# Performance work log

Hardware: AMD Instinct MI355X
Metric: run time of the kernel (lower is better)

The kernel has to match this reference:

```python
import jax, jax.numpy as jnp
import numpy as np
from jax import lax

H = W = 1024

def _conv_sig(x, w, b):
    # 3x3 conv, padding=1 (SAME), NCHW / OIHW, followed by sigmoid
    y = lax.conv_general_dilated(x, w, (1, 1), 'SAME',
                                 dimension_numbers=('NCHW', 'OIHW', 'NCHW'))
    return jax.nn.sigmoid(y + b[None, :, None, None])


def setup_inputs() -> dict:
    key = jax.random.key(0)
    ks = jax.random.split(key, 20)
    d = {
        'x':  jax.random.normal(ks[0], (1, 3, H, W), jnp.float32),
        'x2': jax.random.normal(ks[1], (1, 3, H, W), jnp.float32),
        'w1a': jax.random.normal(ks[2], (1, 3, 3, 3), jnp.float32) * 0.1,
        'b1a': jax.random.normal(ks[3], (1,), jnp.float32) * 0.1,
        'w2a': jax.random.normal(ks[4], (1, 4, 3, 3), jnp.float32) * 0.1,
        'b2a': jax.random.normal(ks[5], (1,), jnp.float32) * 0.1,
        'w3a': jax.random.normal(ks[6], (1, 5, 3, 3), jnp.float32) * 0.1,
        'b3a': jax.random.normal(ks[7], (1,), jnp.float32) * 0.1,
        'w1b': jax.random.normal(ks[8], (1, 3, 3, 3), jnp.float32) * 0.1,
        'b1b': jax.random.normal(ks[9], (1,), jnp.float32) * 0.1,
        'w2b': jax.random.normal(ks[10], (1, 4, 3, 3), jnp.float32) * 0.1,
        'b2b': jax.random.normal(ks[11], (1,), jnp.float32) * 0.1,
        'w3b': jax.random.normal(ks[12], (1, 5, 3, 3), jnp.float32) * 0.1,
        'b3b': jax.random.normal(ks[13], (1,), jnp.float32) * 0.1,
        'lw1': jax.random.normal(ks[14], (128, 6), jnp.float32) * 0.1,
        'lb1': jax.random.normal(ks[15], (128,), jnp.float32) * 0.1,
        'lw2': jax.random.normal(ks[16], (2, 128), jnp.float32) * 0.1,
        'lb2': jax.random.normal(ks[17], (2,), jnp.float32) * 0.1,
    }
    return d


def _encode(x, params):
    # three stacked conv(3x3)+sigmoid blocks with densenet-style concat: C 3->4->5->6
    (w1, b1), (w2, b2), (w3, b3) = params
    x = jnp.concatenate([x, _conv_sig(x, w1, b1)], axis=1)
    x = jnp.concatenate([x, _conv_sig(x, w2, b2)], axis=1)
    x = jnp.concatenate([x, _conv_sig(x, w3, b3)], axis=1)
    return x  # [1, 6, H, W]


def reference(x, x2, w1a, b1a, w2a, b2a, w3a, b3a,
              w1b, b1b, w2b, b2b, w3b, b3b, lw1, lb1, lw2, lb2):
    # name branch: passthrough (3-channel input, e.g. name='opt')
    xa = _encode(x,  [(w1a, b1a), (w2a, b2a), (w3a, b3a)])
    xb = _encode(x2, [(w1b, b1b), (w2b, b2b), (w3b, b3b)])
    x3 = xa - xb                                   # [1, 6, H, W]
    feat = jnp.transpose(x3, (0, 2, 3, 1)).reshape(H * W, 6)
    feat = feat @ lw1.T + lb1                      # [HW, 128]
    outfeature = feat @ lw2.T + lb2                # [HW, 2]
    den_x1 = jnp.transpose(xa, (0, 2, 3, 1)).reshape(H, W, 6)
    den_x2 = jnp.transpose(xb, (0, 2, 3, 1)).reshape(H, W, 6)
    return outfeature, den_x1, den_x2
```

## Files before the change

### kernel.cpp

```cpp
#include <hip/hip_runtime.h>
#include <math.h>

#define IMG  1024
#define TS   32
#define HALO 3
#define XT   38
#define S1T  36
#define S2T  34

__device__ __forceinline__ float sigf(float y) {
    return 1.0f / (1.0f + __expf(-y));
}

__device__ __forceinline__ void acc9(float acc[4], const float v[6][3], const float* w9) {
#pragma unroll
    for (int dy = 0; dy < 3; ++dy)
#pragma unroll
        for (int dx = 0; dx < 3; ++dx) {
            float ww = w9[dy * 3 + dx];
#pragma unroll
            for (int rr = 0; rr < 4; ++rr)
                acc[rr] += ww * v[rr + dy][dx];
        }
}

__global__ __launch_bounds__(256, 4)
void unet_fused(const float* __restrict__ x, const float* __restrict__ x2,
                const float* __restrict__ w1a, const float* __restrict__ b1a,
                const float* __restrict__ w2a, const float* __restrict__ b2a,
                const float* __restrict__ w3a, const float* __restrict__ b3a,
                const float* __restrict__ w1b, const float* __restrict__ b1b,
                const float* __restrict__ w2b, const float* __restrict__ b2b,
                const float* __restrict__ w3b, const float* __restrict__ b3b,
                const float* __restrict__ lw1, const float* __restrict__ lb1,
                const float* __restrict__ lw2, const float* __restrict__ lb2,
                float* __restrict__ out)
{
    __shared__ float xt[3][XT * XT];
    __shared__ float s1[S1T * S1T];
    __shared__ float s2[S2T * S2T];
    __shared__ float wc[14];

    const int tid = threadIdx.x;
    const int bx = blockIdx.x, by = blockIdx.y;
    const int row0 = by * TS - HALO, col0 = bx * TS - HALO;

    const int c_out = tid & 31;
    const int r0_out = (tid >> 5) * 4;

    if (tid < 12) {
        int o = tid / 6, ch = tid % 6;
        float acc = 0.0f;
        for (int k = 0; k < 128; ++k) acc += lw2[o * 128 + k] * lw1[k * 6 + ch];
        wc[tid] = acc;
    } else if (tid < 14) {
        int o = tid - 12;
        float acc = lb2[o];
        for (int k = 0; k < 128; ++k) acc += lw2[o * 128 + k] * lb1[k];
        wc[tid] = acc;
    }

    const float* XS[2] = {x, x2};
    const float* W1[2] = {w1a, w1b};
    const float* W2[2] = {w2a, w2b};
    const float* W3[2] = {w3a, w3b};
    const float* B1[2] = {b1a, b1b};
    const float* B2[2] = {b2a, b2b};
    const float* B3[2] = {b3a, b3b};

    const long out1 = (long)2 * IMG * IMG;
    const long out2 = out1 + (long)6 * IMG * IMG;

    float areg[4][6];

#pragma unroll
    for (int br = 0; br < 2; ++br) {
        const float* xin = XS[br];
        for (int idx = tid; idx < 3 * XT * XT; idx += 256) {
            int pl = idx / (XT * XT);
            int i  = idx - pl * (XT * XT);
            int r = i / XT, cc = i - r * XT;
            int gr = row0 + r, gc = col0 + cc;
            bool ok = ((unsigned)gr < (unsigned)IMG) && ((unsigned)gc < (unsigned)IMG);
            float v = 0.0f;
            if (ok) v = xin[(long)pl * (IMG * IMG) + (long)gr * IMG + gc];
            xt[pl][i] = v;
        }
        __syncthreads();

        {
            float w[27];
#pragma unroll
            for (int i = 0; i < 27; ++i) w[i] = W1[br][i];
            const float bias = B1[br][0];
            for (int item = tid; item < S1T * 9; item += 256) {
                int c = item % S1T, rg = item / S1T;
                int r0 = rg * 4;
                float acc[4] = {bias, bias, bias, bias};
#pragma unroll
                for (int ic = 0; ic < 3; ++ic) {
                    const float* xp = &xt[ic][r0 * XT + c];
                    float v[6][3];
#pragma unroll
                    for (int rr = 0; rr < 6; ++rr)
#pragma unroll
                        for (int cc = 0; cc < 3; ++cc)
                            v[rr][cc] = xp[rr * XT + cc];
                    acc9(acc, v, &w[ic * 9]);
                }
                int gc1 = col0 + 1 + c;
                bool cok = (unsigned)gc1 < (unsigned)IMG;
                float* so = &s1[r0 * S1T + c];
#pragma unroll
                for (int rr = 0; rr < 4; ++rr) {
                    int gr1 = row0 + 1 + r0 + rr;
                    bool ok = cok && ((unsigned)gr1 < (unsigned)IMG);
                    so[rr * S1T] = ok ? sigf(acc[rr]) : 0.0f;
                }
            }
        }
        __syncthreads();

        {
            float w[36];
#pragma unroll
            for (int i = 0; i < 36; ++i) w[i] = W2[br][i];
            const float bias = B2[br][0];
            for (int item = tid; item < S2T * 9; item += 256) {
                int c = item % S2T, rg = item / S2T;
                int r0 = rg * 4;
                float acc[4] = {bias, bias, bias, bias};
#pragma unroll
                for (int ic = 0; ic < 3; ++ic) {
                    float v[6][3];
#pragma unroll
                    for (int rr = 0; rr < 6; ++rr) {
                        int rrow = r0 + 1 + rr; if (rrow > XT - 1) rrow = XT - 1;
#pragma unroll
                        for (int cc = 0; cc < 3; ++cc)
                            v[rr][cc] = xt[ic][rrow * XT + (c + 1 + cc)];
                    }
                    acc9(acc, v, &w[ic * 9]);
                }
                {
                    float v[6][3];
#pragma unroll
                    for (int rr = 0; rr < 6; ++rr) {
                        int rrow = r0 + rr; if (rrow > S1T - 1) rrow = S1T - 1;
#pragma unroll
                        for (int cc = 0; cc < 3; ++cc)
                            v[rr][cc] = s1[rrow * S1T + (c + cc)];
                    }
                    acc9(acc, v, &w[27]);
                }
                int gc2 = col0 + 2 + c;
                bool cok = (unsigned)gc2 < (unsigned)IMG;
                float* so = &s2[r0 * S2T + c];
#pragma unroll
                for (int rr = 0; rr < 4; ++rr) {
                    int srow = r0 + rr;
                    if (srow < S2T) {
                        int gr2 = row0 + 2 + srow;
                        bool ok = cok && ((unsigned)gr2 < (unsigned)IMG);
                        so[rr * S2T] = ok ? sigf(acc[rr]) : 0.0f;
                    }
                }
            }
        }
        __syncthreads();

        {
            float w[45];
#pragma unroll
            for (int i = 0; i < 45; ++i) w[i] = W3[br][i];
            const float bias = B3[br][0];
            const int c = c_out, r0 = r0_out;
            float acc[4] = {bias, bias, bias, bias};
#pragma unroll
            for (int ic = 0; ic < 3; ++ic) {
                float v[6][3];
#pragma unroll
                for (int rr = 0; rr < 6; ++rr)
#pragma unroll
                    for (int cc = 0; cc < 3; ++cc)
                        v[rr][cc] = xt[ic][(r0 + 2 + rr) * XT + (c + 2 + cc)];
                acc9(acc, v, &w[ic * 9]);
            }
            {
                float v[6][3];
#pragma unroll
                for (int rr = 0; rr < 6; ++rr)
#pragma unroll
                    for (int cc = 0; cc < 3; ++cc)
                        v[rr][cc] = s1[(r0 + 1 + rr) * S1T + (c + 1 + cc)];
                acc9(acc, v, &w[27]);
            }
            {
                float v[6][3];
#pragma unroll
                for (int rr = 0; rr < 6; ++rr)
#pragma unroll
                    for (int cc = 0; cc < 3; ++cc)
                        v[rr][cc] = s2[(r0 + rr) * S2T + (c + cc)];
                acc9(acc, v, &w[36]);
            }

            float cur[4][6];
#pragma unroll
            for (int rr = 0; rr < 4; ++rr) {
#pragma unroll
                for (int ch = 0; ch < 3; ++ch)
                    cur[rr][ch] = xt[ch][(r0 + 3 + rr) * XT + (c + 3)];
                cur[rr][3] = s1[(r0 + 2 + rr) * S1T + (c + 2)];
                cur[rr][4] = s2[(r0 + 1 + rr) * S2T + (c + 1)];
                cur[rr][5] = sigf(acc[rr]);
            }

            const long denOff = (br == 0) ? out1 : out2;
#pragma unroll
            for (int rr = 0; rr < 4; ++rr) {
                long gr = (long)by * TS + r0 + rr;
                long pix = gr * IMG + ((long)bx * TS + c);
                float* pd = out + denOff + pix * 6;
#pragma unroll
                for (int ch = 0; ch < 6; ++ch) pd[ch] = cur[rr][ch];
            }

            if (br == 0) {
#pragma unroll
                for (int rr = 0; rr < 4; ++rr)
#pragma unroll
                    for (int ch = 0; ch < 6; ++ch) areg[rr][ch] = cur[rr][ch];
            } else {
                float wcr[14];
#pragma unroll
                for (int i = 0; i < 14; ++i) wcr[i] = wc[i];
#pragma unroll
                for (int rr = 0; rr < 4; ++rr) {
                    float o0 = wcr[12], o1 = wcr[13];
#pragma unroll
                    for (int ch = 0; ch < 6; ++ch) {
                        float d = areg[rr][ch] - cur[rr][ch];
                        o0 += wcr[ch]     * d;
                        o1 += wcr[6 + ch] * d;
                    }
                    long gr = (long)by * TS + r0 + rr;
                    long pix = gr * IMG + ((long)bx * TS + c);
                    out[pix * 2]     = o0;
                    out[pix * 2 + 1] = o1;
                }
            }
        }
        __syncthreads();
    }
}

extern "C" void kernel_launch(void* const* d_in, const int* in_sizes, int n_in,
                              void* d_out, int out_size, void* d_ws, size_t ws_size,
                              hipStream_t stream) {
    const float* x   = (const float*)d_in[0];
    const float* x2  = (const float*)d_in[1];
    const float* w1a = (const float*)d_in[2];
    const float* b1a = (const float*)d_in[3];
    const float* w2a = (const float*)d_in[4];
    const float* b2a = (const float*)d_in[5];
    const float* w3a = (const float*)d_in[6];
    const float* b3a = (const float*)d_in[7];
    const float* w1b = (const float*)d_in[8];
    const float* b1b = (const float*)d_in[9];
    const float* w2b = (const float*)d_in[10];
    const float* b2b = (const float*)d_in[11];
    const float* w3b = (const float*)d_in[12];
    const float* b3b = (const float*)d_in[13];
    const float* lw1 = (const float*)d_in[14];
    const float* lb1 = (const float*)d_in[15];
    const float* lw2 = (const float*)d_in[16];
    const float* lb2 = (const float*)d_in[17];
    float* out = (float*)d_out;

    dim3 grid(IMG / TS, IMG / TS);
    unet_fused<<<grid, 256, 0, stream>>>(x, x2,
                                         w1a, b1a, w2a, b2a, w3a, b3a,
                                         w1b, b1b, w2b, b2b, w3b, b3b,
                                         lw1, lb1, lw2, lb2, out);
}
```

Before: 155.7 us.

## Give each wavefront private conv1/conv2 halo tiles to drop block barriers

Each of the four wavefronts now computes its own 12-row conv1 and 10-row conv2 strips, with the halo rows recomputed, in per-wave shared buffers. This removes the block-wide __syncthreads between the conv stages. The convs now use a sliding row window that reuses each loaded row across three output rows instead of reloading 6x3 patches. The branch-0 features are reduced straight to the two projected partial sums, which frees registers. The cost is redundant halo compute and idle lanes: only 36 and 34 of the 64 lanes are active in stages 1 and 2.

```diff
diff --git a/kernel.cpp b/kernel.cpp
--- a/kernel.cpp
+++ b/kernel.cpp
@@ -1,28 +1,17 @@
 #include <hip/hip_runtime.h>
-#include <math.h>
 
 #define IMG  1024
 #define TS   32
-#define HALO 3
 #define XT   38
-#define S1T  36
-#define S2T  34
-
-__device__ __forceinline__ float sigf(float y) {
-    return 1.0f / (1.0f + __expf(-y));
-}
-
-__device__ __forceinline__ void acc9(float acc[4], const float v[6][3], const float* w9) {
-#pragma unroll
-    for (int dy = 0; dy < 3; ++dy)
-#pragma unroll
-        for (int dx = 0; dx < 3; ++dx) {
-            float ww = w9[dy * 3 + dx];
-#pragma unroll
-            for (int rr = 0; rr < 4; ++rr)
-                acc[rr] += ww * v[rr + dy][dx];
-        }
-}
+#define XTA  (XT*XT)
+#define S1R  12
+#define S1C  36
+#define S2R  10
+#define S2C  34
+#define OUT1 (2*IMG*IMG)
+#define OUT2 (OUT1 + 6*IMG*IMG)
+
+__device__ __forceinline__ float sigf(float y) { return 1.0f / (1.0f + __expf(-y)); }
 
 __global__ __launch_bounds__(256, 4)
 void unet_fused(const float* __restrict__ x, const float* __restrict__ x2,
@@ -36,20 +25,18 @@
                 const float* __restrict__ lw2, const float* __restrict__ lb2,
                 float* __restrict__ out)
 {
-    __shared__ float xt[3][XT * XT];
-    __shared__ float s1[S1T * S1T];
-    __shared__ float s2[S2T * S2T];
+    __shared__ float xt[3][XTA];
+    __shared__ float s1[4][S1R * S1C];
+    __shared__ float s2[4][S2R * S2C];
     __shared__ float wc[14];
 
-    const int tid = threadIdx.x;
-    const int bx = blockIdx.x, by = blockIdx.y;
-    const int row0 = by * TS - HALO, col0 = bx * TS - HALO;
-
-    const int c_out = tid & 31;
-    const int r0_out = (tid >> 5) * 4;
+    const int tid  = threadIdx.x;
+    const int wv   = tid >> 6;
+    const int lane = tid & 63;
+    const int R0 = blockIdx.y * TS, C0 = blockIdx.x * TS;
 
     if (tid < 12) {
-        int o = tid / 6, ch = tid % 6;
+        int o = tid / 6, ch = tid - o * 6;
         float acc = 0.0f;
         for (int k = 0; k < 128; ++k) acc += lw2[o * 128 + k] * lw1[k * 6 + ch];
         wc[tid] = acc;
@@ -68,190 +55,217 @@
     const float* B2[2] = {b2a, b2b};
     const float* B3[2] = {b3a, b3b};
 
-    const long out1 = (long)2 * IMG * IMG;
-    const long out2 = out1 + (long)6 * IMG * IMG;
-
-    float areg[4][6];
+    float pa[4][2];
+    float* s1w = s1[wv];
+    float* s2w = s2[wv];
+
+    const int c_out = lane & 31;
+    const int rg    = lane >> 5;
+    const int tr0   = 8 * wv + rg * 4;
 
 #pragma unroll
     for (int br = 0; br < 2; ++br) {
+        __syncthreads();
         const float* xin = XS[br];
-        for (int idx = tid; idx < 3 * XT * XT; idx += 256) {
-            int pl = idx / (XT * XT);
-            int i  = idx - pl * (XT * XT);
-            int r = i / XT, cc = i - r * XT;
-            int gr = row0 + r, gc = col0 + cc;
-            bool ok = ((unsigned)gr < (unsigned)IMG) && ((unsigned)gc < (unsigned)IMG);
+        for (int it = tid; it < 3 * XTA; it += 256) {
+            int ch = it / XTA, rem = it - ch * XTA;
+            int r = rem / XT, c = rem - r * XT;
+            int gr = R0 - 3 + r, gc = C0 - 3 + c;
             float v = 0.0f;
-            if (ok) v = xin[(long)pl * (IMG * IMG) + (long)gr * IMG + gc];
-            xt[pl][i] = v;
+            if ((unsigned)gr < (unsigned)IMG && (unsigned)gc < (unsigned)IMG)
+                v = xin[ch * (IMG * IMG) + gr * IMG + gc];
+            xt[ch][rem] = v;
         }
         __syncthreads();
 
+        if (lane < S1C) {
+            const int sc = lane;
+            const float b1 = B1[br][0];
+            float acc[S1R];
+#pragma unroll
+            for (int q = 0; q < S1R; ++q) acc[q] = b1;
+#pragma unroll
+            for (int ch = 0; ch < 3; ++ch) {
+                float w9[9];
+#pragma unroll
+                for (int i = 0; i < 9; ++i) w9[i] = W1[br][ch * 9 + i];
+                const float* xp = &xt[ch][(8 * wv) * XT + sc];
+#pragma unroll
+                for (int r = 0; r < 14; ++r) {
+                    float a0 = xp[0], a1 = xp[1], a2 = xp[2];
+                    xp += XT;
+#pragma unroll
+                    for (int dy = 0; dy < 3; ++dy) {
+                        int q = r - dy;
+                        if (q >= 0 && q < S1R)
+                            acc[q] += w9[dy * 3] * a0 + w9[dy * 3 + 1] * a1 + w9[dy * 3 + 2] * a2;
+                    }
+                }
+            }
+            const int gcol = C0 - 2 + sc;
+            const bool cok = (unsigned)gcol < (unsigned)IMG;
+            const int grow0 = R0 + 8 * wv - 2;
+#pragma unroll
+            for (int q = 0; q < S1R; ++q) {
+                bool ok = cok && ((unsigned)(grow0 + q) < (unsigned)IMG);
+                s1w[q * S1C + sc] = ok ? sigf(acc[q]) : 0.0f;
+            }
+        }
+
+        if (lane < S2C) {
+            const int sc = lane;
+            const float b2 = B2[br][0];
+            float acc[S2R];
+#pragma unroll
+            for (int q = 0; q < S2R; ++q) acc[q] = b2;
+#pragma unroll
+            for (int ch = 0; ch < 3; ++ch) {
+                float w9[9];
+#pragma unroll
+                for (int i = 0; i < 9; ++i) w9[i] = W2[br][ch * 9 + i];
+                const float* xp = &xt[ch][(8 * wv + 1) * XT + (sc + 1)];
+#pragma unroll
+                for (int r = 0; r < 12; ++r) {
+                    float a0 = xp[0], a1 = xp[1], a2 = xp[2];
+                    xp += XT;
+#pragma unroll
+                    for (int dy = 0; dy < 3; ++dy) {
+                        int q = r - dy;
+                        if (q >= 0 && q < S2R)
+                            acc[q] += w9[dy * 3] * a0 + w9[dy * 3 + 1] * a1 + w9[dy * 3 + 2] * a2;
+                    }
+                }
+            }
+            {
+                float w9[9];
+#pragma unroll
+                for (int i = 0; i < 9; ++i) w9[i] = W2[br][27 + i];
+                const float* sp = &s1w[sc];
+#pragma unroll
+                for (int r = 0; r < 12; ++r) {
+                    float a0 = sp[0], a1 = sp[1], a2 = sp[2];
+                    sp += S1C;
+#pragma unroll
+                    for (int dy = 0; dy < 3; ++dy) {
+                        int q = r - dy;
+                        if (q >= 0 && q < S2R)
+                            acc[q] += w9[dy * 3] * a0 + w9[dy * 3 + 1] * a1 + w9[dy * 3 + 2] * a2;
+                    }
+                }
+            }
+            const int gcol = C0 - 1 + sc;
+            const bool cok = (unsigned)gcol < (unsigned)IMG;
+            const int grow0 = R0 + 8 * wv - 1;
+#pragma unroll
+            for (int q = 0; q < S2R; ++q) {
+                bool ok = cok && ((unsigned)(grow0 + q) < (unsigned)IMG);
+                s2w[q * S2C + sc] = ok ? sigf(acc[q]) : 0.0f;
+            }
+        }
+
         {
-            float w[27];
-#pragma unroll
-            for (int i = 0; i < 27; ++i) w[i] = W1[br][i];
-            const float bias = B1[br][0];
-            for (int item = tid; item < S1T * 9; item += 256) {
-                int c = item % S1T, rg = item / S1T;
-                int r0 = rg * 4;
-                float acc[4] = {bias, bias, bias, bias};
-#pragma unroll
-                for (int ic = 0; ic < 3; ++ic) {
-                    const float* xp = &xt[ic][r0 * XT + c];
-                    float v[6][3];
-#pragma unroll
-                    for (int rr = 0; rr < 6; ++rr)
-#pragma unroll
-                        for (int cc = 0; cc < 3; ++cc)
-                            v[rr][cc] = xp[rr * XT + cc];
-                    acc9(acc, v, &w[ic * 9]);
-                }
-                int gc1 = col0 + 1 + c;
-                bool cok = (unsigned)gc1 < (unsigned)IMG;
-                float* so = &s1[r0 * S1T + c];
+            const int c = c_out;
+            const float b3v = B3[br][0];
+            float acc[4] = {b3v, b3v, b3v, b3v};
+#pragma unroll
+            for (int ch = 0; ch < 3; ++ch) {
+                float w9[9];
+#pragma unroll
+                for (int i = 0; i < 9; ++i) w9[i] = W3[br][ch * 9 + i];
+                const float* xp = &xt[ch][(tr0 + 2) * XT + (c + 2)];
+#pragma unroll
+                for (int r = 0; r < 6; ++r) {
+                    float a0 = xp[0], a1 = xp[1], a2 = xp[2];
+                    xp += XT;
+#pragma unroll
+                    for (int dy = 0; dy < 3; ++dy) {
+                        int q = r - dy;
+                        if (q >= 0 && q < 4)
+                            acc[q] += w9[dy * 3] * a0 + w9[dy * 3 + 1] * a1 + w9[dy * 3 + 2] * a2;
+                    }
+                }
+            }
+            {
+                float w9[9];
+#pragma unroll
+                for (int i = 0; i < 9; ++i) w9[i] = W3[br][27 + i];
+                const float* sp = &s1w[(rg * 4 + 1) * S1C + (c + 1)];
+#pragma unroll
+                for (int r = 0; r < 6; ++r) {
+                    float a0 = sp[0], a1 = sp[1], a2 = sp[2];
+                    sp += S1C;
+#pragma unroll
+                    for (int dy = 0; dy < 3; ++dy) {
+                        int q = r - dy;
+                        if (q >= 0 && q < 4)
+                            acc[q] += w9[dy * 3] * a0 + w9[dy * 3 + 1] * a1 + w9[dy * 3 + 2] * a2;
+                    }
+                }
+            }
+            {
+                float w9[9];
+#pragma unroll
+                for (int i = 0; i < 9; ++i) w9[i] = W3[br][36 + i];
+                const float* sp = &s2w[(rg * 4) * S2C + c];
+#pragma unroll
+                for (int r = 0; r < 6; ++r) {
+                    float a0 = sp[0], a1 = sp[1], a2 = sp[2];
+                    sp += S2C;
+#pragma unroll
+                    for (int dy = 0; dy < 3; ++dy) {
+                        int q = r - dy;
+                        if (q >= 0 && q < 4)
+                            acc[q] += w9[dy * 3] * a0 + w9[dy * 3 + 1] * a1 + w9[dy * 3 + 2] * a2;
+                    }
+                }
+            }
+
+            float cur[4][6];
+#pragma unroll
+            for (int rr = 0; rr < 4; ++rr) {
+#pragma unroll
+                for (int ch = 0; ch < 3; ++ch)
+                    cur[rr][ch] = xt[ch][(tr0 + 3 + rr) * XT + (c + 3)];
+                cur[rr][3] = s1w[(rg * 4 + 2 + rr) * S1C + (c + 2)];
+                cur[rr][4] = s2w[(rg * 4 + 1 + rr) * S2C + (c + 1)];
+                cur[rr][5] = sigf(acc[rr]);
+            }
+
+            const int denOff = (br == 0) ? OUT1 : OUT2;
+#pragma unroll
+            for (int rr = 0; rr < 4; ++rr) {
+                int pix = (R0 + tr0 + rr) * IMG + C0 + c;
+                float* pd = out + denOff + pix * 6;
+#pragma unroll
+                for (int ch = 0; ch < 6; ++ch) pd[ch] = cur[rr][ch];
+            }
+            if (br == 0) {
 #pragma unroll
                 for (int rr = 0; rr < 4; ++rr) {
-                    int gr1 = row0 + 1 + r0 + rr;
-                    bool ok = cok && ((unsigned)gr1 < (unsigned)IMG);
-                    so[rr * S1T] = ok ? sigf(acc[rr]) : 0.0f;
-                }
-            }
-        }
-        __syncthreads();
-
-        {
-            float w[36];
-#pragma unroll
-            for (int i = 0; i < 36; ++i) w[i] = W2[br][i];
-            const float bias = B2[br][0];
-            for (int item = tid; item < S2T * 9; item += 256) {
-                int c = item % S2T, rg = item / S2T;
-                int r0 = rg * 4;
-                float acc[4] = {bias, bias, bias, bias};
-#pragma unroll
-                for (int ic = 0; ic < 3; ++ic) {
-                    float v[6][3];
-#pragma unroll
-                    for (int rr = 0; rr < 6; ++rr) {
-                        int rrow = r0 + 1 + rr; if (rrow > XT - 1) rrow = XT - 1;
-#pragma unroll
-                        for (int cc = 0; cc < 3; ++cc)
-                            v[rr][cc] = xt[ic][rrow * XT + (c + 1 + cc)];
-                    }
-                    acc9(acc, v, &w[ic * 9]);
-                }
-                {
-                    float v[6][3];
-#pragma unroll
-                    for (int rr = 0; rr < 6; ++rr) {
-                        int rrow = r0 + rr; if (rrow > S1T - 1) rrow = S1T - 1;
-#pragma unroll
-                        for (int cc = 0; cc < 3; ++cc)
-                            v[rr][cc] = s1[rrow * S1T + (c + cc)];
-                    }
-                    acc9(acc, v, &w[27]);
-                }
-                int gc2 = col0 + 2 + c;
-                bool cok = (unsigned)gc2 < (unsigned)IMG;
-                float* so = &s2[r0 * S2T + c];
+                    float p0 = 0.0f, p1 = 0.0f;
+#pragma unroll
+                    for (int ch = 0; ch < 6; ++ch) {
+                        p0 += wc[ch]     * cur[rr][ch];
+                        p1 += wc[6 + ch] * cur[rr][ch];
+                    }
+                    pa[rr][0] = p0; pa[rr][1] = p1;
+                }
+            } else {
 #pragma unroll
                 for (int rr = 0; rr < 4; ++rr) {
-                    int srow = r0 + rr;
-                    if (srow < S2T) {
-                        int gr2 = row0 + 2 + srow;
-                        bool ok = cok && ((unsigned)gr2 < (unsigned)IMG);
-                        so[rr * S2T] = ok ? sigf(acc[rr]) : 0.0f;
-                    }
-                }
-            }
-        }
-        __syncthreads();
-
-        {
-            float w[45];
-#pragma unroll
-            for (int i = 0; i < 45; ++i) w[i] = W3[br][i];
-            const float bias = B3[br][0];
-            const int c = c_out, r0 = r0_out;
-            float acc[4] = {bias, bias, bias, bias};
-#pragma unroll
-            for (int ic = 0; ic < 3; ++ic) {
-                float v[6][3];
-#pragma unroll
-                for (int rr = 0; rr < 6; ++rr)
-#pragma unroll
-                    for (int cc = 0; cc < 3; ++cc)
-                        v[rr][cc] = xt[ic][(r0 + 2 + rr) * XT + (c + 2 + cc)];
-                acc9(acc, v, &w[ic * 9]);
-            }
-            {
-                float v[6][3];
-#pragma unroll
-                for (int rr = 0; rr < 6; ++rr)
-#pragma unroll
-                    for (int cc = 0; cc < 3; ++cc)
-                        v[rr][cc] = s1[(r0 + 1 + rr) * S1T + (c + 1 + cc)];
-                acc9(acc, v, &w[27]);
-            }
-            {
-                float v[6][3];
-#pragma unroll
-                for (int rr = 0; rr < 6; ++rr)
-#pragma unroll
-                    for (int cc = 0; cc < 3; ++cc)
-                        v[rr][cc] = s2[(r0 + rr) * S2T + (c + cc)];
-                acc9(acc, v, &w[36]);
-            }
-
-            float cur[4][6];
-#pragma unroll
-            for (int rr = 0; rr < 4; ++rr) {
-#pragma unroll
-                for (int ch = 0; ch < 3; ++ch)
-                    cur[rr][ch] = xt[ch][(r0 + 3 + rr) * XT + (c + 3)];
-                cur[rr][3] = s1[(r0 + 2 + rr) * S1T + (c + 2)];
-                cur[rr][4] = s2[(r0 + 1 + rr) * S2T + (c + 1)];
-                cur[rr][5] = sigf(acc[rr]);
-            }
-
-            const long denOff = (br == 0) ? out1 : out2;
-#pragma unroll
-            for (int rr = 0; rr < 4; ++rr) {
-                long gr = (long)by * TS + r0 + rr;
-                long pix = gr * IMG + ((long)bx * TS + c);
-                float* pd = out + denOff + pix * 6;
-#pragma unroll
-                for (int ch = 0; ch < 6; ++ch) pd[ch] = cur[rr][ch];
-            }
-
-            if (br == 0) {
-#pragma unroll
-                for (int rr = 0; rr < 4; ++rr)
-#pragma unroll
-                    for (int ch = 0; ch < 6; ++ch) areg[rr][ch] = cur[rr][ch];
-            } else {
-                float wcr[14];
-#pragma unroll
-                for (int i = 0; i < 14; ++i) wcr[i] = wc[i];
-#pragma unroll
-                for (int rr = 0; rr < 4; ++rr) {
-                    float o0 = wcr[12], o1 = wcr[13];
+                    float o0 = pa[rr][0] + wc[12];
+                    float o1 = pa[rr][1] + wc[13];
 #pragma unroll
                     for (int ch = 0; ch < 6; ++ch) {
-                        float d = areg[rr][ch] - cur[rr][ch];
-                        o0 += wcr[ch]     * d;
-                        o1 += wcr[6 + ch] * d;
-                    }
-                    long gr = (long)by * TS + r0 + rr;
-                    long pix = gr * IMG + ((long)bx * TS + c);
+                        o0 -= wc[ch]     * cur[rr][ch];
+                        o1 -= wc[6 + ch] * cur[rr][ch];
+                    }
+                    int pix = (R0 + tr0 + rr) * IMG + C0 + c;
                     out[pix * 2]     = o0;
                     out[pix * 2 + 1] = o1;
                 }
             }
         }
-        __syncthreads();
     }
 }
 
```

New measurement: 233.8 us. +50.2%, slower.
